# Kernel optimization log

Hardware: AMD Instinct MI355X
Metric: run time of the kernel (lower is better)

Reference implementation:

```python
import jax, jax.numpy as jnp
import numpy as np

NUM_VOXELS = 1_000_000
N_POINTS = 1_500_000
TOTAL_PROP_PTS = 1_000_000
NUM_PROPOSALS = 2048
IN_CH = 134  # 3 + 3 + 128
M = 16       # backbone output width
BATCH = 8


def setup_inputs() -> dict:
    key = jax.random.key(0)
    k1, k2, k3, k4, k5, k6 = jax.random.split(key, 6)
    voxel_feats = jax.random.normal(k1, (NUM_VOXELS, IN_CH), dtype=jnp.float32)
    W = jax.random.normal(k2, (IN_CH, M), dtype=jnp.float32) * 0.05
    p2v_map = jax.random.randint(k3, (N_POINTS,), 0, NUM_VOXELS, dtype=jnp.int64)
    # column 0: proposal id (unused), column 1: point index into pt_feats
    col1 = jax.random.randint(k4, (TOTAL_PROP_PTS,), 0, N_POINTS, dtype=jnp.int64)
    gt_proposals_idx = jnp.stack([jnp.zeros_like(col1), col1], axis=1)
    interior = jnp.sort(jax.random.randint(k5, (NUM_PROPOSALS - 1,), 0, TOTAL_PROP_PTS, dtype=jnp.int64))
    gt_proposals_offset = jnp.concatenate([
        jnp.zeros((1,), jnp.int64), interior,
        jnp.full((1,), TOTAL_PROP_PTS, jnp.int64)])
    # column 0 is the batch (scene) id
    locs_scaled = jax.random.randint(k6, (N_POINTS, 4), 0, BATCH, dtype=jnp.int32)
    return {
        'voxel_feats': voxel_feats,
        'W': W,
        'p2v_map': p2v_map,
        'gt_proposals_idx': gt_proposals_idx,
        'gt_proposals_offset': gt_proposals_offset,
        'locs_scaled': locs_scaled,
    }


def reference(voxel_feats, W, p2v_map, gt_proposals_idx, gt_proposals_offset, locs_scaled):
    # Stand-in for the Minkowski sparse backbone: pointwise projection + ReLU, 134 -> 16.
    feats = jax.nn.relu(voxel_feats @ W)                 # (V, 16)
    pt_feats = feats[p2v_map]                            # (N, 16) voxel->point gather

    P = gt_proposals_offset.shape[0] - 1
    point_idx = gt_proposals_idx[:, 1]                   # (T,)
    T = point_idx.shape[0]

    # CSR offsets -> segment ids (replaces the Python loop over proposals)
    seg_ids = jnp.searchsorted(gt_proposals_offset, jnp.arange(T), side='right') - 1

    gathered = pt_feats[point_idx]                       # (T, 16) ragged gather
    sums = jax.ops.segment_sum(gathered, seg_ids, num_segments=P)
    counts = jax.ops.segment_sum(jnp.ones((T,), feats.dtype), seg_ids, num_segments=P)
    proposal_feats = sums / jnp.maximum(counts, 1.0)[:, None]   # (P, 16) segment mean

    batch_idxs = locs_scaled[:, 0]                       # (N,) scene ids
    proposals_batchId = batch_idxs[point_idx][gt_proposals_offset[:-1]]  # (P,)
    proposal_objectness_scores = jnp.ones((P,), dtype=bool)
    return proposal_feats, proposals_batchId, proposal_objectness_scores
```

## Files before the change

kernel.cpp:

```cpp
#include <hip/hip_runtime.h>

#define NUM_VOXELS     1000000
#define N_POINTS       1500000
#define TOTAL_PROP_PTS 1000000
#define NUM_PROPOSALS  2048
#define IN_CH          134
#define M_OUT          16

__global__ __launch_bounds__(256, 4) void k_gemm_relu(
    const float* __restrict__ A, const float* __restrict__ W,
    float* __restrict__ feats)
{
    __shared__ float lds[4][64 * 33];
    const int wave = threadIdx.x >> 6;
    const int lane = threadIdx.x & 63;
    const int v0   = blockIdx.x * 256 + wave * 64;
    if (v0 >= NUM_VOXELS) return;

    float* chunk = lds[wave];

    const float* myrow = A + (size_t)(v0 + lane) * IN_CH;
    const float2 tl0 = *(const float2*)(myrow + 128);
    const float2 tl1 = *(const float2*)(myrow + 130);
    const float2 tl2 = *(const float2*)(myrow + 132);

    const int srow = lane >> 4;
    const int scol = (lane & 15) * 2;
    const float* sbase = A + (size_t)(v0 + srow) * IN_CH + scol;

    float2 buf[16];
#pragma unroll
    for (int j = 0; j < 16; ++j)
        buf[j] = *(const float2*)(sbase + (size_t)j * 4 * IN_CH);

    float acc[M_OUT];
#pragma unroll
    for (int c = 0; c < M_OUT; ++c) acc[c] = 0.f;

#pragma unroll
    for (int cidx = 0; cidx < 4; ++cidx) {
        const int kc = cidx * 32;

#pragma unroll
        for (int j = 0; j < 16; ++j) {
            const int row = j * 4 + srow;
            *(float2*)&chunk[row * 33 + scol] = buf[j];
        }

        if (cidx < 3) {
            const float* nb = sbase + kc + 32;
#pragma unroll
            for (int j = 0; j < 16; ++j)
                buf[j] = *(const float2*)(nb + (size_t)j * 4 * IN_CH);
        }

        const float* wbase = W + kc * M_OUT;
#pragma unroll
        for (int kk = 0; kk < 32; ++kk) {
            const float a = chunk[lane * 33 + kk];
            const float* wr = wbase + kk * M_OUT;
#pragma unroll
            for (int c = 0; c < M_OUT; ++c) acc[c] = fmaf(a, wr[c], acc[c]);
        }
    }

    {
        const float* wr = W + 128 * M_OUT;
#pragma unroll
        for (int c = 0; c < M_OUT; ++c) {
            float v = fmaf(tl0.x, wr[0 * M_OUT + c], acc[c]);
            v = fmaf(tl0.y, wr[1 * M_OUT + c], v);
            v = fmaf(tl1.x, wr[2 * M_OUT + c], v);
            v = fmaf(tl1.y, wr[3 * M_OUT + c], v);
            v = fmaf(tl2.x, wr[4 * M_OUT + c], v);
            acc[c] = fmaf(tl2.y, wr[5 * M_OUT + c], v);
        }
    }

    float4* orow = (float4*)(feats + (size_t)(v0 + lane) * M_OUT);
#pragma unroll
    for (int q = 0; q < 4; ++q) {
        float4 o;
        o.x = fmaxf(acc[q * 4 + 0], 0.f);
        o.y = fmaxf(acc[q * 4 + 1], 0.f);
        o.z = fmaxf(acc[q * 4 + 2], 0.f);
        o.w = fmaxf(acc[q * 4 + 3], 0.f);
        orow[q] = o;
    }
}

__global__ __launch_bounds__(256) void k_propmean(
    const float* __restrict__ feats,
    const int*   __restrict__ p2v,
    const int*   __restrict__ prop_idx,
    const int*   __restrict__ offsets,
    const int*   __restrict__ locs,
    float*       __restrict__ out)
{
    const int s   = blockIdx.x;
    const int tid = threadIdx.x;
    const int t0  = offsets[s];
    const int t1  = offsets[s + 1];
    const int2* pidx2 = (const int2*)prop_idx;

    float acc[M_OUT];
#pragma unroll
    for (int c = 0; c < M_OUT; ++c) acc[c] = 0.f;

    int t = t0 + tid;
    bool have = (t < t1);
    int v = 0;
    if (have) v = p2v[pidx2[t].y];

    while (have) {
        const int  tn     = t + 256;
        const bool have_n = (tn < t1);
        int vn = 0;
        if (have_n) vn = p2v[pidx2[tn].y];

        const float4* fp = (const float4*)(feats + (size_t)v * M_OUT);
        const float4 f0 = fp[0], f1 = fp[1], f2 = fp[2], f3 = fp[3];
        acc[0]  += f0.x; acc[1]  += f0.y; acc[2]  += f0.z; acc[3]  += f0.w;
        acc[4]  += f1.x; acc[5]  += f1.y; acc[6]  += f1.z; acc[7]  += f1.w;
        acc[8]  += f2.x; acc[9]  += f2.y; acc[10] += f2.z; acc[11] += f2.w;
        acc[12] += f3.x; acc[13] += f3.y; acc[14] += f3.z; acc[15] += f3.w;

        v = vn; t = tn; have = have_n;
    }

#pragma unroll
    for (int c = 0; c < M_OUT; ++c) {
#pragma unroll
        for (int off = 32; off > 0; off >>= 1)
            acc[c] += __shfl_down(acc[c], off, 64);
    }

    __shared__ float red[4][M_OUT];
    const int lane = tid & 63, wv = tid >> 6;
    if (lane == 0) {
#pragma unroll
        for (int c = 0; c < M_OUT; ++c) red[wv][c] = acc[c];
    }
    __syncthreads();

    if (tid < M_OUT) {
        const float sum = red[0][tid] + red[1][tid] + red[2][tid] + red[3][tid];
        const float cnt = (float)(t1 - t0);
        out[s * M_OUT + tid] = sum / fmaxf(cnt, 1.f);
    }
    if (tid == 0) {
        const int p = prop_idx[2 * t0 + 1];
        out[NUM_PROPOSALS * M_OUT + s]                 = (float)locs[4 * p];
        out[NUM_PROPOSALS * M_OUT + NUM_PROPOSALS + s] = 1.0f;
    }
}

extern "C" void kernel_launch(void* const* d_in, const int* in_sizes, int n_in,
                              void* d_out, int out_size, void* d_ws, size_t ws_size,
                              hipStream_t stream)
{
    const float* A    = (const float*)d_in[0];
    const float* W    = (const float*)d_in[1];
    const int*   p2v  = (const int*)  d_in[2];
    const int*   pidx = (const int*)  d_in[3];
    const int*   offs = (const int*)  d_in[4];
    const int*   locs = (const int*)  d_in[5];
    float*       out  = (float*)      d_out;
    float*       feats = (float*)     d_ws;

    k_gemm_relu<<<(NUM_VOXELS + 255) / 256, 256, 0, stream>>>(A, W, feats);
    k_propmean<<<NUM_PROPOSALS, 256, 0, stream>>>(feats, p2v, pidx, offs, locs, out);
}
```

Before: 774.3 us.

## Precompute proposal voxel indices inside GEMM launch and use quad-lane float4 gathers

Extra blocks are added to the GEMM kernel that resolve each proposal point's voxel index (p2v[prop_idx]) into a workspace array, so this dependent double-indirection runs alongside the GEMM rather than inside the segment-mean kernel. The mean kernel now assigns four lanes per point, each loading one float4 of the 16-wide feature row, which gives coalesced 64-byte accesses and fewer accumulator registers. The cost is an extra 4 MB write and read of the index array, plus a changed reduction layout.

```diff
diff --git a/kernel.cpp b/kernel.cpp
--- a/kernel.cpp
+++ b/kernel.cpp
@@ -7,10 +7,23 @@
 #define IN_CH          134
 #define M_OUT          16
 
-__global__ __launch_bounds__(256, 4) void k_gemm_relu(
+#define G1 ((NUM_VOXELS + 255) / 256)
+#define GV ((TOTAL_PROP_PTS + 255) / 256)
+
+__global__ __launch_bounds__(256, 4) void k_gemm_relu_vt(
     const float* __restrict__ A, const float* __restrict__ W,
-    float* __restrict__ feats)
+    const int* __restrict__ p2v, const int* __restrict__ prop_idx,
+    float* __restrict__ feats, int* __restrict__ vt)
 {
+    if (blockIdx.x >= G1) {
+        const int t = (blockIdx.x - G1) * 256 + threadIdx.x;
+        if (t < TOTAL_PROP_PTS) {
+            const int2* pidx2 = (const int2*)prop_idx;
+            vt[t] = p2v[pidx2[t].y];
+        }
+        return;
+    }
+
     __shared__ float lds[4][64 * 33];
     const int wave = threadIdx.x >> 6;
     const int lane = threadIdx.x & 63;
@@ -40,20 +53,17 @@
 #pragma unroll
     for (int cidx = 0; cidx < 4; ++cidx) {
         const int kc = cidx * 32;
-
 #pragma unroll
         for (int j = 0; j < 16; ++j) {
             const int row = j * 4 + srow;
             *(float2*)&chunk[row * 33 + scol] = buf[j];
         }
-
         if (cidx < 3) {
             const float* nb = sbase + kc + 32;
 #pragma unroll
             for (int j = 0; j < 16; ++j)
                 buf[j] = *(const float2*)(nb + (size_t)j * 4 * IN_CH);
         }
-
         const float* wbase = W + kc * M_OUT;
 #pragma unroll
         for (int kk = 0; kk < 32; ++kk) {
@@ -63,7 +73,6 @@
             for (int c = 0; c < M_OUT; ++c) acc[c] = fmaf(a, wr[c], acc[c]);
         }
     }
-
     {
         const float* wr = W + 128 * M_OUT;
 #pragma unroll
@@ -76,7 +85,6 @@
             acc[c] = fmaf(tl2.y, wr[5 * M_OUT + c], v);
         }
     }
-
     float4* orow = (float4*)(feats + (size_t)(v0 + lane) * M_OUT);
 #pragma unroll
     for (int q = 0; q < 4; ++q) {
@@ -91,7 +99,7 @@
 
 __global__ __launch_bounds__(256) void k_propmean(
     const float* __restrict__ feats,
-    const int*   __restrict__ p2v,
+    const int*   __restrict__ vt,
     const int*   __restrict__ prop_idx,
     const int*   __restrict__ offsets,
     const int*   __restrict__ locs,
@@ -101,50 +109,44 @@
     const int tid = threadIdx.x;
     const int t0  = offsets[s];
     const int t1  = offsets[s + 1];
-    const int2* pidx2 = (const int2*)prop_idx;
+    const int g   = tid >> 2;
+    const int q   = tid & 3;
 
-    float acc[M_OUT];
-#pragma unroll
-    for (int c = 0; c < M_OUT; ++c) acc[c] = 0.f;
+    float a0 = 0.f, a1 = 0.f, a2 = 0.f, a3 = 0.f;
 
-    int t = t0 + tid;
-    bool have = (t < t1);
-    int v = 0;
-    if (have) v = p2v[pidx2[t].y];
+    int t = t0 + g;
+    int v = (t < t1) ? vt[t] : -1;
 
-    while (have) {
-        const int  tn     = t + 256;
-        const bool have_n = (tn < t1);
-        int vn = 0;
-        if (have_n) vn = p2v[pidx2[tn].y];
+    for (int base = t0; base < t1; base += 64) {
+        const int tn = t + 64;
+        const int vn = (tn < t1) ? vt[tn] : -1;
 
-        const float4* fp = (const float4*)(feats + (size_t)v * M_OUT);
-        const float4 f0 = fp[0], f1 = fp[1], f2 = fp[2], f3 = fp[3];
-        acc[0]  += f0.x; acc[1]  += f0.y; acc[2]  += f0.z; acc[3]  += f0.w;
-        acc[4]  += f1.x; acc[5]  += f1.y; acc[6]  += f1.z; acc[7]  += f1.w;
-        acc[8]  += f2.x; acc[9]  += f2.y; acc[10] += f2.z; acc[11] += f2.w;
-        acc[12] += f3.x; acc[13] += f3.y; acc[14] += f3.z; acc[15] += f3.w;
-
-        v = vn; t = tn; have = have_n;
+        if (v >= 0) {
+            const float4 f = *(const float4*)(feats + (size_t)v * M_OUT + q * 4);
+            a0 += f.x; a1 += f.y; a2 += f.z; a3 += f.w;
+        }
+        v = vn; t = tn;
     }
 
 #pragma unroll
-    for (int c = 0; c < M_OUT; ++c) {
-#pragma unroll
-        for (int off = 32; off > 0; off >>= 1)
-            acc[c] += __shfl_down(acc[c], off, 64);
+    for (int off = 4; off < 64; off <<= 1) {
+        a0 += __shfl_down(a0, off, 64);
+        a1 += __shfl_down(a1, off, 64);
+        a2 += __shfl_down(a2, off, 64);
+        a3 += __shfl_down(a3, off, 64);
     }
 
-    __shared__ float red[4][M_OUT];
+    __shared__ float red[4][4][4];
     const int lane = tid & 63, wv = tid >> 6;
-    if (lane == 0) {
-#pragma unroll
-        for (int c = 0; c < M_OUT; ++c) red[wv][c] = acc[c];
+    if (lane < 4) {
+        red[wv][lane][0] = a0; red[wv][lane][1] = a1;
+        red[wv][lane][2] = a2; red[wv][lane][3] = a3;
     }
     __syncthreads();
 
     if (tid < M_OUT) {
-        const float sum = red[0][tid] + red[1][tid] + red[2][tid] + red[3][tid];
+        const float sum = red[0][tid >> 2][tid & 3] + red[1][tid >> 2][tid & 3]
+                        + red[2][tid >> 2][tid & 3] + red[3][tid >> 2][tid & 3];
         const float cnt = (float)(t1 - t0);
         out[s * M_OUT + tid] = sum / fmaxf(cnt, 1.f);
     }
@@ -166,8 +168,10 @@
     const int*   offs = (const int*)  d_in[4];
     const int*   locs = (const int*)  d_in[5];
     float*       out  = (float*)      d_out;
-    float*       feats = (float*)     d_ws;
 
-    k_gemm_relu<<<(NUM_VOXELS + 255) / 256, 256, 0, stream>>>(A, W, feats);
-    k_propmean<<<NUM_PROPOSALS, 256, 0, stream>>>(feats, p2v, pidx, offs, locs, out);
+    float* feats = (float*)d_ws;
+    int*   vt    = (int*)((char*)d_ws + (size_t)64 * 1024 * 1024);
+
+    k_gemm_relu_vt<<<G1 + GV, 256, 0, stream>>>(A, W, p2v, pidx, feats, vt);
+    k_propmean<<<NUM_PROPOSALS, 256, 0, stream>>>(feats, vt, pidx, offs, locs, out);
 }
```

Result: no change. 777.9 us (+0.5%).
